# Optimization experiments

Hardware: AMD Instinct MI355X
Metric: run time of the kernel (lower is better)

The kernel has to match this reference:

```python
import jax, jax.numpy as jnp
import numpy as np

T = 10.0
DIVISOR = 3.0
K = 2
LAMBDA_ALPHA = 1.0
LAMBDA_BETA = 0.5


def setup_inputs() -> dict:
    key = jax.random.key(0)
    ks = jax.random.split(key, 5)
    N, C, H, W = 32, 64, 112, 112
    R = 8
    hidden = C // R
    x = jax.random.normal(ks[0], (N, C, H, W), dtype=jnp.float32)
    conv_w = jax.random.normal(ks[1], (C,), dtype=jnp.float32) * 0.1
    conv_b = jnp.zeros((1,), dtype=jnp.float32)
    w1 = jax.random.normal(ks[2], (C, hidden), dtype=jnp.float32) * 0.1
    b1 = jnp.zeros((hidden,), dtype=jnp.float32)
    w2 = jax.random.normal(ks[3], (hidden, 2 * K * C), dtype=jnp.float32) * 0.1
    b2 = jnp.zeros((2 * K * C,), dtype=jnp.float32)
    return {"x": x, "conv_w": conv_w, "conv_b": conv_b,
            "w1": w1, "b1": b1, "w2": w2, "b2": b2}


def reference(x, conv_w, conv_b, w1, b1, w2, b2):
    N, C, H, W = x.shape
    gamma = (H * W) / DIVISOR

    # Spatial attention: 1x1 conv C->1, per-sample softmax over HW, scale+clamp.
    s = jnp.einsum('nchw,c->nhw', x, conv_w) + conv_b[0]          # [N,H,W]
    p = jax.nn.softmax((s / T).reshape(N, -1), axis=-1)            # [N,HW]
    spatial = jnp.minimum(gamma * p, 1.0).reshape(N, 1, H, W)      # [N,1,H,W]

    # Residual head (DyReLU-C coefficient branch): GAP -> FC -> ReLU -> FC -> 2*sigmoid-1.
    pooled = x.mean(axis=(2, 3))                                   # [N,C]
    h = jax.nn.relu(pooled @ w1 + b1)                              # [N,C//R]
    theta = 2.0 * jax.nn.sigmoid(h @ w2 + b2) - 1.0                # [N,2*K*C]
    theta = theta.reshape(N, K, C, 2)
    alpha = theta[..., 0]                                          # [N,K,C]
    beta = theta[..., 1]                                           # [N,K,C]

    init_alpha = jnp.array([1.0, 0.0], dtype=x.dtype)              # K=2
    init_beta = jnp.array([1.0, 0.0], dtype=x.dtype)
    a = init_alpha[None, :, None] + LAMBDA_ALPHA * alpha           # [N,K,C]
    b = init_beta[None, :, None] + LAMBDA_BETA * beta              # [N,K,C]

    # result_k = spatial * (x * a_k + b_k); max over k branches.
    out_k = spatial[:, None] * (x[:, None] * a[..., None, None] + b[..., None, None])
    return jnp.max(out_k, axis=1)                                  # [N,C,H,W]
```

## Files before the change

kernel.cpp:

```cpp
#include <hip/hip_runtime.h>
#include <math.h>

#define NN 32
#define CC 64
#define HWD 12544
#define HW4 3136
#define HID 8
#define OUTD 256
#define T_INV 0.1f
#define GAMMA_F (12544.0f / 3.0f)

__device__ __forceinline__ float wave_sum(float v) {
    #pragma unroll
    for (int off = 32; off; off >>= 1) v += __shfl_down(v, off, 64);
    return v;
}
__device__ __forceinline__ float wave_max(float v) {
    #pragma unroll
    for (int off = 32; off; off >>= 1) v = fmaxf(v, __shfl_down(v, off, 64));
    return v;
}

__global__ __launch_bounds__(256) void k_conv(const float* __restrict__ x,
                                              const float* __restrict__ cw,
                                              const float* __restrict__ cb,
                                              float* __restrict__ s) {
    __shared__ float w[CC];
    int tid = threadIdx.x;
    if (tid < CC) w[tid] = cw[tid];
    __syncthreads();
    int g = blockIdx.x * 256 + tid;
    int n = g / HW4;
    int r = g - n * HW4;
    const float4* x4 = (const float4*)x;
    float4 acc = make_float4(0.f, 0.f, 0.f, 0.f);
    long base = (long)(n * CC) * HW4 + r;
    #pragma unroll 8
    for (int c = 0; c < CC; c++) {
        float4 v = x4[base + (long)c * HW4];
        float ww = w[c];
        acc.x += v.x * ww; acc.y += v.y * ww;
        acc.z += v.z * ww; acc.w += v.w * ww;
    }
    float bb = cb[0];
    acc.x += bb; acc.y += bb; acc.z += bb; acc.w += bb;
    ((float4*)s)[g] = acc;
}

__global__ __launch_bounds__(256) void k_pool(const float* __restrict__ x,
                                              float* __restrict__ pooled) {
    int bid = blockIdx.x;
    const float4* x4 = (const float4*)x + (long)bid * HW4;
    float acc = 0.f;
    for (int i = threadIdx.x; i < HW4; i += 256) {
        float4 v = x4[i];
        acc += (v.x + v.y) + (v.z + v.w);
    }
    acc = wave_sum(acc);
    __shared__ float lds[4];
    int lane = threadIdx.x & 63, wv = threadIdx.x >> 6;
    if (lane == 0) lds[wv] = acc;
    __syncthreads();
    if (threadIdx.x == 0) {
        pooled[bid] = (lds[0] + lds[1] + lds[2] + lds[3]) * (1.0f / HWD);
    }
}

__global__ __launch_bounds__(256) void k_softmax(float* __restrict__ s) {
    int n = blockIdx.x;
    float4* s4 = (float4*)s + (long)n * HW4;
    int tid = threadIdx.x;
    int lane = tid & 63, wv = tid >> 6;
    __shared__ float lds[4];
    __shared__ float bcast;

    float vmax = -3.4e38f;
    for (int i = tid; i < HW4; i += 256) {
        float4 v = s4[i];
        vmax = fmaxf(vmax, fmaxf(fmaxf(v.x, v.y), fmaxf(v.z, v.w)));
    }
    vmax = wave_max(vmax);
    if (lane == 0) lds[wv] = vmax;
    __syncthreads();
    if (tid == 0) bcast = fmaxf(fmaxf(lds[0], lds[1]), fmaxf(lds[2], lds[3]));
    __syncthreads();
    float m = bcast;
    __syncthreads();

    float acc = 0.f;
    for (int i = tid; i < HW4; i += 256) {
        float4 v = s4[i];
        acc += __expf((v.x - m) * T_INV) + __expf((v.y - m) * T_INV)
             + __expf((v.z - m) * T_INV) + __expf((v.w - m) * T_INV);
    }
    acc = wave_sum(acc);
    if (lane == 0) lds[wv] = acc;
    __syncthreads();
    if (tid == 0) bcast = lds[0] + lds[1] + lds[2] + lds[3];
    __syncthreads();
    float scale = GAMMA_F / bcast;

    for (int i = tid; i < HW4; i += 256) {
        float4 v = s4[i];
        v.x = fminf(scale * __expf((v.x - m) * T_INV), 1.f);
        v.y = fminf(scale * __expf((v.y - m) * T_INV), 1.f);
        v.z = fminf(scale * __expf((v.z - m) * T_INV), 1.f);
        v.w = fminf(scale * __expf((v.w - m) * T_INV), 1.f);
        s4[i] = v;
    }
}

__global__ __launch_bounds__(256) void k_mlp(const float* __restrict__ pooled,
                                             const float* __restrict__ w1,
                                             const float* __restrict__ b1,
                                             const float* __restrict__ w2,
                                             const float* __restrict__ b2,
                                             float* __restrict__ a_ws,
                                             float* __restrict__ b_ws) {
    int n = blockIdx.x, t = threadIdx.x;
    __shared__ float p[CC];
    __shared__ float h[HID];
    if (t < CC) p[t] = pooled[n * CC + t];
    __syncthreads();
    if (t < HID) {
        float acc = b1[t];
        #pragma unroll 8
        for (int c = 0; c < CC; c++) acc += p[c] * w1[c * HID + t];
        h[t] = fmaxf(acc, 0.f);
    }
    __syncthreads();
    float o = b2[t];
    #pragma unroll
    for (int j = 0; j < HID; j++) o += h[j] * w2[j * OUTD + t];
    float theta = 2.f / (1.f + __expf(-o)) - 1.f;
    int k = t >> 7;
    int c = (t >> 1) & 63;
    int d = t & 1;
    float init = (k == 0) ? 1.f : 0.f;
    int idx = n * 128 + k * 64 + c;
    if (d == 0) a_ws[idx] = init + theta;
    else        b_ws[idx] = init + 0.5f * theta;
}

__global__ __launch_bounds__(256) void k_final(const float* __restrict__ x,
                                               const float* __restrict__ sp,
                                               const float* __restrict__ a_ws,
                                               const float* __restrict__ b_ws,
                                               float* __restrict__ out) {
    int bid = blockIdx.x;
    int n = bid >> 6, c = bid & 63;
    float a0 = a_ws[n * 128 + c];
    float b0 = b_ws[n * 128 + c];
    float a1 = a_ws[n * 128 + 64 + c];
    float b1v = b_ws[n * 128 + 64 + c];
    const float4* x4 = (const float4*)x + (long)bid * HW4;
    const float4* sp4 = (const float4*)sp + (long)n * HW4;
    float4* o4 = (float4*)out + (long)bid * HW4;
    for (int i = threadIdx.x; i < HW4; i += 256) {
        float4 xv = x4[i];
        float4 sv = sp4[i];
        float4 r;
        r.x = sv.x * fmaxf(xv.x * a0 + b0, xv.x * a1 + b1v);
        r.y = sv.y * fmaxf(xv.y * a0 + b0, xv.y * a1 + b1v);
        r.z = sv.z * fmaxf(xv.z * a0 + b0, xv.z * a1 + b1v);
        r.w = sv.w * fmaxf(xv.w * a0 + b0, xv.w * a1 + b1v);
        o4[i] = r;
    }
}

extern "C" void kernel_launch(void* const* d_in, const int* in_sizes, int n_in,
                              void* d_out, int out_size, void* d_ws, size_t ws_size,
                              hipStream_t stream) {
    const float* x      = (const float*)d_in[0];
    const float* conv_w = (const float*)d_in[1];
    const float* conv_b = (const float*)d_in[2];
    const float* w1     = (const float*)d_in[3];
    const float* b1     = (const float*)d_in[4];
    const float* w2     = (const float*)d_in[5];
    const float* b2     = (const float*)d_in[6];
    float* out = (float*)d_out;

    float* ws = (float*)d_ws;
    float* s      = ws;
    float* pooled = s + NN * HWD;
    float* a_ws   = pooled + NN * CC;
    float* b_ws   = a_ws + NN * 2 * CC;

    k_conv   <<<(NN * HW4) / 256, 256, 0, stream>>>(x, conv_w, conv_b, s);
    k_pool   <<<NN * CC,          256, 0, stream>>>(x, pooled);
    k_softmax<<<NN,               256, 0, stream>>>(s);
    k_mlp    <<<NN,               256, 0, stream>>>(pooled, w1, b1, w2, b2, a_ws, b_ws);
    k_final  <<<NN * CC,          256, 0, stream>>>(x, s, a_ws, b_ws, out);
}
```

Before: 240.5 us.

## Fuse conv with pooling and fold softmax normalization into final kernel

Merges the 1x1 conv and the global average pool into one kernel, so x is read once for both. Each block writes partial channel sums and partial exp-sums for its slice of HW, and the MLP kernel reduces them. The separate softmax kernel is removed: the final kernel recomputes exp(s/T), scaled by a per-sample factor, and the output store is now nontemporal. Two risks: the max-subtraction is dropped, so large logits could overflow. Per-channel wave shuffle reductions inside the conv loop, plus an uneven tail over HW pieces, add compute to the fused kernel.

```diff
diff --git a/kernel.cpp b/kernel.cpp
--- a/kernel.cpp
+++ b/kernel.cpp
@@ -9,118 +9,82 @@
 #define OUTD 256
 #define T_INV 0.1f
 #define GAMMA_F (12544.0f / 3.0f)
+#define BPN 12
+
+typedef float v4f __attribute__((ext_vector_type(4)));
 
 __device__ __forceinline__ float wave_sum(float v) {
     #pragma unroll
     for (int off = 32; off; off >>= 1) v += __shfl_down(v, off, 64);
     return v;
 }
-__device__ __forceinline__ float wave_max(float v) {
-    #pragma unroll
-    for (int off = 32; off; off >>= 1) v = fmaxf(v, __shfl_down(v, off, 64));
-    return v;
+
+__global__ __launch_bounds__(256) void k1_conv_pool(const float* __restrict__ x,
+        const float* __restrict__ cw, const float* __restrict__ cb,
+        float* __restrict__ s, float* __restrict__ pp, float* __restrict__ se) {
+    __shared__ float w[CC];
+    __shared__ float pool_lds[4][CC];
+    __shared__ float se_lds[4];
+    int tid = threadIdx.x;
+    int n = blockIdx.x / BPN, piece = blockIdx.x % BPN;
+    if (tid < CC) w[tid] = cw[tid];
+    pool_lds[tid >> 6][tid & 63] = 0.f;
+    __syncthreads();
+    int lane = tid & 63, wv = tid >> 6;
+    const float4* x4 = (const float4*)x + (long)n * CC * HW4;
+    float4* s4 = (float4*)s + (long)n * HW4;
+    float bb = cb[0];
+    float se_acc = 0.f;
+    for (int i = piece * 256 + tid; i < HW4; i += BPN * 256) {
+        float4 acc = make_float4(0.f, 0.f, 0.f, 0.f);
+        #pragma unroll 8
+        for (int c = 0; c < CC; c++) {
+            float4 v = x4[(long)c * HW4 + i];
+            float ww = w[c];
+            acc.x += v.x * ww; acc.y += v.y * ww;
+            acc.z += v.z * ww; acc.w += v.w * ww;
+            float pv = (v.x + v.y) + (v.z + v.w);
+            pv = wave_sum(pv);
+            if (lane == 0) pool_lds[wv][c] += pv;
+        }
+        acc.x += bb; acc.y += bb; acc.z += bb; acc.w += bb;
+        s4[i] = acc;
+        se_acc += __expf(acc.x * T_INV) + __expf(acc.y * T_INV)
+                + __expf(acc.z * T_INV) + __expf(acc.w * T_INV);
+    }
+    se_acc = wave_sum(se_acc);
+    if (lane == 0) se_lds[wv] = se_acc;
+    __syncthreads();
+    if (tid < CC) {
+        float p = pool_lds[0][tid] + pool_lds[1][tid]
+                + pool_lds[2][tid] + pool_lds[3][tid];
+        pp[(n * BPN + piece) * CC + tid] = p;
+    }
+    if (tid == 0)
+        se[n * BPN + piece] = se_lds[0] + se_lds[1] + se_lds[2] + se_lds[3];
 }
 
-__global__ __launch_bounds__(256) void k_conv(const float* __restrict__ x,
-                                              const float* __restrict__ cw,
-                                              const float* __restrict__ cb,
-                                              float* __restrict__ s) {
-    __shared__ float w[CC];
-    int tid = threadIdx.x;
-    if (tid < CC) w[tid] = cw[tid];
-    __syncthreads();
-    int g = blockIdx.x * 256 + tid;
-    int n = g / HW4;
-    int r = g - n * HW4;
-    const float4* x4 = (const float4*)x;
-    float4 acc = make_float4(0.f, 0.f, 0.f, 0.f);
-    long base = (long)(n * CC) * HW4 + r;
-    #pragma unroll 8
-    for (int c = 0; c < CC; c++) {
-        float4 v = x4[base + (long)c * HW4];
-        float ww = w[c];
-        acc.x += v.x * ww; acc.y += v.y * ww;
-        acc.z += v.z * ww; acc.w += v.w * ww;
-    }
-    float bb = cb[0];
-    acc.x += bb; acc.y += bb; acc.z += bb; acc.w += bb;
-    ((float4*)s)[g] = acc;
-}
-
-__global__ __launch_bounds__(256) void k_pool(const float* __restrict__ x,
-                                              float* __restrict__ pooled) {
-    int bid = blockIdx.x;
-    const float4* x4 = (const float4*)x + (long)bid * HW4;
-    float acc = 0.f;
-    for (int i = threadIdx.x; i < HW4; i += 256) {
-        float4 v = x4[i];
-        acc += (v.x + v.y) + (v.z + v.w);
-    }
-    acc = wave_sum(acc);
-    __shared__ float lds[4];
-    int lane = threadIdx.x & 63, wv = threadIdx.x >> 6;
-    if (lane == 0) lds[wv] = acc;
-    __syncthreads();
-    if (threadIdx.x == 0) {
-        pooled[bid] = (lds[0] + lds[1] + lds[2] + lds[3]) * (1.0f / HWD);
-    }
-}
-
-__global__ __launch_bounds__(256) void k_softmax(float* __restrict__ s) {
-    int n = blockIdx.x;
-    float4* s4 = (float4*)s + (long)n * HW4;
-    int tid = threadIdx.x;
-    int lane = tid & 63, wv = tid >> 6;
-    __shared__ float lds[4];
-    __shared__ float bcast;
-
-    float vmax = -3.4e38f;
-    for (int i = tid; i < HW4; i += 256) {
-        float4 v = s4[i];
-        vmax = fmaxf(vmax, fmaxf(fmaxf(v.x, v.y), fmaxf(v.z, v.w)));
-    }
-    vmax = wave_max(vmax);
-    if (lane == 0) lds[wv] = vmax;
-    __syncthreads();
-    if (tid == 0) bcast = fmaxf(fmaxf(lds[0], lds[1]), fmaxf(lds[2], lds[3]));
-    __syncthreads();
-    float m = bcast;
-    __syncthreads();
-
-    float acc = 0.f;
-    for (int i = tid; i < HW4; i += 256) {
-        float4 v = s4[i];
-        acc += __expf((v.x - m) * T_INV) + __expf((v.y - m) * T_INV)
-             + __expf((v.z - m) * T_INV) + __expf((v.w - m) * T_INV);
-    }
-    acc = wave_sum(acc);
-    if (lane == 0) lds[wv] = acc;
-    __syncthreads();
-    if (tid == 0) bcast = lds[0] + lds[1] + lds[2] + lds[3];
-    __syncthreads();
-    float scale = GAMMA_F / bcast;
-
-    for (int i = tid; i < HW4; i += 256) {
-        float4 v = s4[i];
-        v.x = fminf(scale * __expf((v.x - m) * T_INV), 1.f);
-        v.y = fminf(scale * __expf((v.y - m) * T_INV), 1.f);
-        v.z = fminf(scale * __expf((v.z - m) * T_INV), 1.f);
-        v.w = fminf(scale * __expf((v.w - m) * T_INV), 1.f);
-        s4[i] = v;
-    }
-}
-
-__global__ __launch_bounds__(256) void k_mlp(const float* __restrict__ pooled,
-                                             const float* __restrict__ w1,
-                                             const float* __restrict__ b1,
-                                             const float* __restrict__ w2,
-                                             const float* __restrict__ b2,
-                                             float* __restrict__ a_ws,
-                                             float* __restrict__ b_ws) {
+__global__ __launch_bounds__(256) void k2_mlp(const float* __restrict__ pp,
+        const float* __restrict__ se, const float* __restrict__ w1,
+        const float* __restrict__ b1, const float* __restrict__ w2,
+        const float* __restrict__ b2, float* __restrict__ a_ws,
+        float* __restrict__ b_ws, float* __restrict__ scale) {
     int n = blockIdx.x, t = threadIdx.x;
     __shared__ float p[CC];
     __shared__ float h[HID];
-    if (t < CC) p[t] = pooled[n * CC + t];
+    if (t < CC) {
+        float acc = 0.f;
+        #pragma unroll
+        for (int piece = 0; piece < BPN; piece++)
+            acc += pp[(n * BPN + piece) * CC + t];
+        p[t] = acc * (1.0f / HWD);
+    }
+    if (t == 0) {
+        float ss = 0.f;
+        #pragma unroll
+        for (int piece = 0; piece < BPN; piece++) ss += se[n * BPN + piece];
+        scale[n] = GAMMA_F / ss;
+    }
     __syncthreads();
     if (t < HID) {
         float acc = b1[t];
@@ -133,38 +97,41 @@
     #pragma unroll
     for (int j = 0; j < HID; j++) o += h[j] * w2[j * OUTD + t];
     float theta = 2.f / (1.f + __expf(-o)) - 1.f;
-    int k = t >> 7;
-    int c = (t >> 1) & 63;
-    int d = t & 1;
+    int k = t >> 7, c = (t >> 1) & 63, d = t & 1;
     float init = (k == 0) ? 1.f : 0.f;
     int idx = n * 128 + k * 64 + c;
     if (d == 0) a_ws[idx] = init + theta;
     else        b_ws[idx] = init + 0.5f * theta;
 }
 
-__global__ __launch_bounds__(256) void k_final(const float* __restrict__ x,
-                                               const float* __restrict__ sp,
-                                               const float* __restrict__ a_ws,
-                                               const float* __restrict__ b_ws,
-                                               float* __restrict__ out) {
+__global__ __launch_bounds__(256) void k3_final(const float* __restrict__ x,
+        const float* __restrict__ s, const float* __restrict__ a_ws,
+        const float* __restrict__ b_ws, const float* __restrict__ scale,
+        float* __restrict__ out) {
     int bid = blockIdx.x;
     int n = bid >> 6, c = bid & 63;
     float a0 = a_ws[n * 128 + c];
     float b0 = b_ws[n * 128 + c];
     float a1 = a_ws[n * 128 + 64 + c];
     float b1v = b_ws[n * 128 + 64 + c];
+    float sc = scale[n];
     const float4* x4 = (const float4*)x + (long)bid * HW4;
-    const float4* sp4 = (const float4*)sp + (long)n * HW4;
-    float4* o4 = (float4*)out + (long)bid * HW4;
+    const float4* s4 = (const float4*)s + (long)n * HW4;
+    v4f* o4 = (v4f*)out + (long)bid * HW4;
     for (int i = threadIdx.x; i < HW4; i += 256) {
         float4 xv = x4[i];
-        float4 sv = sp4[i];
-        float4 r;
-        r.x = sv.x * fmaxf(xv.x * a0 + b0, xv.x * a1 + b1v);
-        r.y = sv.y * fmaxf(xv.y * a0 + b0, xv.y * a1 + b1v);
-        r.z = sv.z * fmaxf(xv.z * a0 + b0, xv.z * a1 + b1v);
-        r.w = sv.w * fmaxf(xv.w * a0 + b0, xv.w * a1 + b1v);
-        o4[i] = r;
+        float4 sv = s4[i];
+        v4f r;
+        float sp;
+        sp = fminf(sc * __expf(sv.x * T_INV), 1.f);
+        r.x = sp * fmaxf(xv.x * a0 + b0, xv.x * a1 + b1v);
+        sp = fminf(sc * __expf(sv.y * T_INV), 1.f);
+        r.y = sp * fmaxf(xv.y * a0 + b0, xv.y * a1 + b1v);
+        sp = fminf(sc * __expf(sv.z * T_INV), 1.f);
+        r.z = sp * fmaxf(xv.z * a0 + b0, xv.z * a1 + b1v);
+        sp = fminf(sc * __expf(sv.w * T_INV), 1.f);
+        r.w = sp * fmaxf(xv.w * a0 + b0, xv.w * a1 + b1v);
+        __builtin_nontemporal_store(r, &o4[i]);
     }
 }
 
@@ -180,15 +147,15 @@
     const float* b2     = (const float*)d_in[6];
     float* out = (float*)d_out;
 
-    float* ws = (float*)d_ws;
-    float* s      = ws;
-    float* pooled = s + NN * HWD;
-    float* a_ws   = pooled + NN * CC;
-    float* b_ws   = a_ws + NN * 2 * CC;
+    float* ws   = (float*)d_ws;
+    float* s    = ws;
+    float* pp   = s + NN * HWD;
+    float* se   = pp + NN * BPN * CC;
+    float* a_ws = se + NN * BPN;
+    float* b_ws = a_ws + NN * 2 * CC;
+    float* scl  = b_ws + NN * 2 * CC;
 
-    k_conv   <<<(NN * HW4) / 256, 256, 0, stream>>>(x, conv_w, conv_b, s);
-    k_pool   <<<NN * CC,          256, 0, stream>>>(x, pooled);
-    k_softmax<<<NN,               256, 0, stream>>>(s);
-    k_mlp    <<<NN,               256, 0, stream>>>(pooled, w1, b1, w2, b2, a_ws, b_ws);
-    k_final  <<<NN * CC,          256, 0, stream>>>(x, s, a_ws, b_ws, out);
+    k1_conv_pool<<<NN * BPN, 256, 0, stream>>>(x, conv_w, conv_b, s, pp, se);
+    k2_mlp      <<<NN,       256, 0, stream>>>(pp, se, w1, b1, w2, b2, a_ws, b_ws, scl);
+    k3_final    <<<NN * CC,  256, 0, stream>>>(x, s, a_ws, b_ws, scl, out);
 }
```

Result: slower. 276.8 us (+15.1%).
